# Kernel tuning notes

Measured on AMD Instinct MI355X. Metric: run time of the kernel, lower is better.

The kernel has to match this reference:

```python
import jax, jax.numpy as jnp
import numpy as np

B, F, U, H1, H2 = 2048, 256, 64, 64, 32
E = F + 1  # attention embed dim = num_inputs + 1


def setup_inputs() -> dict:
    key = jax.random.key(0)
    ks = jax.random.split(key, 14)
    s = lambda fan: 1.0 / np.sqrt(fan)
    inp = {
        "x": jax.random.normal(ks[0], (B, F), jnp.float32),
        # stacked per-feature FeatureNN params (Linear(1,U) -> Linear(U,H1) -> Linear(H1,H2) -> Linear(H2,1))
        "w1": jax.random.normal(ks[1], (F, U), jnp.float32) * s(1),
        "b1": jnp.zeros((F, U), jnp.float32),
        "w2": jax.random.normal(ks[2], (F, U, H1), jnp.float32) * s(U),
        "b2": jnp.zeros((F, H1), jnp.float32),
        "w3": jax.random.normal(ks[3], (F, H1, H2), jnp.float32) * s(H1),
        "b3": jnp.zeros((F, H2), jnp.float32),
        "w4": jax.random.normal(ks[4], (F, H2), jnp.float32) * s(H2),
        "b4": jnp.zeros((F,), jnp.float32),
        # MultiheadAttention(E, 1) params: packed qkv in_proj + out_proj
        "in_w": jax.random.normal(ks[5], (3 * E, E), jnp.float32) * s(E),
        "in_b": jnp.zeros((3 * E,), jnp.float32),
        "out_w": jax.random.normal(ks[6], (E, E), jnp.float32) * s(E),
        "out_b": jnp.zeros((E,), jnp.float32),
        "bias": jnp.zeros((1,), jnp.float32),
    }
    return inp


def _attention(x, in_w, in_b, out_w, out_b):
    # x: [B, F]; build [B, F, E] = concat(one-hot feature index, value)
    b = x.shape[0]
    eye = jnp.eye(F, dtype=x.dtype)
    xa = jnp.concatenate([jnp.broadcast_to(eye, (b, F, F)), x[:, :, None]], axis=-1)  # [B,F,E]
    qkv = jnp.einsum("bse,fe->bsf", xa, in_w) + in_b  # [B,F,3E]
    q, k, v = jnp.split(qkv, 3, axis=-1)
    scores = jnp.einsum("bqe,bke->bqk", q, k) / jnp.sqrt(jnp.asarray(E, x.dtype))
    attn = jax.nn.softmax(scores, axis=-1)
    ctx = jnp.einsum("bqk,bke->bqe", attn, v)
    out = jnp.einsum("bqe,fe->bqf", ctx, out_w) + out_b  # out_proj
    return out[:, :, -1]  # keep only the value channel -> [B, F]


def _feature_nns(x, w1, b1, w2, b2, w3, b3, w4, b4):
    # x: [B, F] -> per-feature independent MLPs, batched across features
    h = jax.nn.relu(x[:, :, None] * w1[None] + b1[None])          # [B,F,U]
    h = jax.nn.relu(jnp.einsum("bfu,fuh->bfh", h, w2) + b2[None])  # [B,F,H1]
    h = jax.nn.relu(jnp.einsum("bfh,fhg->bfg", h, w3) + b3[None])  # [B,F,H2]
    return jnp.einsum("bfg,fg->bf", h, w4) + b4[None]              # [B,F]


def reference(x, w1, b1, w2, b2, w3, b3, w4, b4, in_w, in_b, out_w, out_b, bias):
    xa = _attention(x, in_w, in_b, out_w, out_b)                   # att_before_flag=True
    fo = _feature_nns(xa, w1, b1, w2, b2, w3, b3, w4, b4)          # dropout is identity (p=0 / eval)
    out = jnp.sum(fo, axis=-1) + bias                              # [B] + bias -> [B]
    return (out, fo)
```

## Files before the change

kernel.cpp:

```cpp
#include <hip/hip_runtime.h>

#define BB 2048
#define FF 256
#define EE 257
#define UU 64
#define HH1 64
#define HH2 32

#define SC 0.089992807f

typedef __attribute__((ext_vector_type(8))) short short8;
typedef __attribute__((ext_vector_type(4))) float f32x4;
typedef __attribute__((ext_vector_type(4))) unsigned u32x4;
typedef __attribute__((ext_vector_type(2))) unsigned u32x2;

#define MF(a, b, c) __builtin_amdgcn_mfma_f32_16x16x32_bf16(a, b, c, 0, 0, 0)
#define EXP2(x) __builtin_amdgcn_exp2f(x)

__device__ inline unsigned cvt_pk(float a, float b) {
    unsigned r;
    asm("v_cvt_pk_bf16_f32 %0, %1, %2" : "=v"(r) : "v"(a), "v"(b));
    return r;
}
struct HiLo { unsigned hi, lo; };
__device__ inline HiLo split2(float a, float b) {
    HiLo r;
    r.hi = cvt_pk(a, b);
    float ha = __builtin_bit_cast(float, r.hi << 16);
    float hb = __builtin_bit_cast(float, r.hi & 0xFFFF0000u);
    r.lo = cvt_pk(a - ha, b - hb);
    return r;
}

__global__ __launch_bounds__(256) void k_prep(const float* __restrict__ in_w,
                                              const float* __restrict__ in_b,
                                              const float* __restrict__ out_w,
                                              const float* __restrict__ out_b,
                                              const float* __restrict__ w2,
                                              const float* __restrict__ w3,
                                              float* __restrict__ mt,
                                              float* __restrict__ uv, float* __restrict__ wgf,
                                              float* __restrict__ sc,
                                              short* __restrict__ w2s, short* __restrict__ w3s) {
    const int blk = blockIdx.x;
    const int t = threadIdx.x;
    __shared__ float red[4][256];
    __shared__ float s0[EE + 3];
    __shared__ float s1[EE + 3];
    if (blk < 256) {
        const int ki = blk;
        for (int j = t; j < EE; j += 256) {
            s0[j] = in_w[(EE + j) * EE + ki] + in_b[EE + j];
            s1[j] = in_b[j];
        }
        __syncthreads();
        const int w = t >> 6, l = t & 63;
        const int j0 = (w * EE) >> 2, j1 = ((w + 1) * EE) >> 2;
        float acc[4] = {0.f, 0.f, 0.f, 0.f};
#pragma unroll 4
        for (int j = j0; j < j1; ++j) {
            float ak = s0[j];
            float bj = s1[j];
#pragma unroll
            for (int g = 0; g < 4; ++g) {
                float aq = in_w[j * EE + l + 64 * g] + bj;
                acc[g] = fmaf(aq, ak, acc[g]);
            }
        }
#pragma unroll
        for (int g = 0; g < 4; ++g) red[w][l + 64 * g] = acc[g];
        __syncthreads();
        {
            float s = red[0][t] + red[1][t] + red[2][t] + red[3][t];
            mt[(ki >> 1) * 512 + t * 2 + (ki & 1)] = s * SC;
        }
    } else if (blk < 512) {
        const int f = blk - 256;
        const int l = t & 63, q = t >> 6;
        const int lr = l & 15, lq = l >> 4;
        const float* w2f = w2 + f * (UU * HH1);
        const float* w3f = w3 + f * (HH1 * HH2);
        short* o2 = w2s + f * 8192;
        short* o3 = w3s + f * 4096;
        const int hperm = (q & 1) * 32 + (lr >> 2) * 8 + ((q >> 1) << 2) + (lr & 3);
#pragma unroll
        for (int kb = 0; kb < 2; ++kb) {
            float v[8];
#pragma unroll
            for (int j = 0; j < 8; ++j) v[j] = w2f[(kb * 32 + lq * 8 + j) * HH1 + hperm];
            u32x4 hi, lo;
#pragma unroll
            for (int p = 0; p < 4; ++p) {
                HiLo s = split2(v[2 * p], v[2 * p + 1]);
                hi[p] = s.hi; lo[p] = s.lo;
            }
            *(short8*)(o2 + ((0 * 2 + kb) * 4 + q) * 512 + l * 8) = __builtin_bit_cast(short8, hi);
            *(short8*)(o2 + ((1 * 2 + kb) * 4 + q) * 512 + l * 8) = __builtin_bit_cast(short8, lo);
        }
        {
            const int kb = q & 1, ct = q >> 1;
            float v[8];
#pragma unroll
            for (int j = 0; j < 8; ++j) v[j] = w3f[(kb * 32 + lq * 8 + j) * HH2 + ct * 16 + lr];
            u32x4 hi, lo;
#pragma unroll
            for (int p = 0; p < 4; ++p) {
                HiLo s = split2(v[2 * p], v[2 * p + 1]);
                hi[p] = s.hi; lo[p] = s.lo;
            }
            *(short8*)(o3 + ((0 * 2 + kb) * 2 + ct) * 512 + l * 8) = __builtin_bit_cast(short8, hi);
            *(short8*)(o3 + ((1 * 2 + kb) * 2 + ct) * 512 + l * 8) = __builtin_bit_cast(short8, lo);
        }
    } else if (blk < 515) {
        const int which = blk - 512;
        for (int j = t; j < EE; j += 256) {
            if (which == 0)      { s0[j] = in_w[(EE + j) * EE + FF];    s1[j] = in_b[j]; }
            else if (which == 1) { s0[j] = in_w[j * EE + FF];           s1[j] = in_b[EE + j]; }
            else                 { s0[j] = out_w[(EE - 1) * EE + j];    s1[j] = in_b[2 * EE + j]; }
        }
        __syncthreads();
        const int w = t >> 6, l = t & 63;
        const int j0 = (w * EE) >> 2, j1 = ((w + 1) * EE) >> 2;
        const int rowbase = which * EE;
        float acc[4] = {0.f, 0.f, 0.f, 0.f};
#pragma unroll 4
        for (int j = j0; j < j1; ++j) {
            float sk = s0[j];
            float bj = s1[j];
#pragma unroll
            for (int g = 0; g < 4; ++g) {
                float av = in_w[(rowbase + j) * EE + l + 64 * g] + bj;
                acc[g] = fmaf(av, sk, acc[g]);
            }
        }
#pragma unroll
        for (int g = 0; g < 4; ++g) red[w][l + 64 * g] = acc[g];
        __syncthreads();
        {
            float s = red[0][t] + red[1][t] + red[2][t] + red[3][t];
            if (which == 0)      uv[t]          = s * SC;
            else if (which == 1) wgf[2 * t]     = s * SC;
            else                 wgf[2 * t + 1] = s;
        }
    } else {
        const int j = t;
        float cq = in_w[j * EE + FF];
        float ck = in_w[(EE + j) * EE + FF];
        float cv = in_w[(2 * EE + j) * EE + FF];
        float rj = out_w[(EE - 1) * EE + j];
        float pa = cq * ck, pb = cv * rj;
        if (t == 0) {
            const int j2 = 256;
            pa += in_w[j2 * EE + FF] * in_w[(EE + j2) * EE + FF];
            pb += in_w[(2 * EE + j2) * EE + FF] * out_w[(EE - 1) * EE + j2];
        }
#pragma unroll
        for (int o = 32; o > 0; o >>= 1) {
            pa += __shfl_down(pa, o, 64);
            pb += __shfl_down(pb, o, 64);
        }
        if ((t & 63) == 0) { red[0][t >> 6] = pa; red[1][t >> 6] = pb; }
        __syncthreads();
        if (t == 0) {
            pa = red[0][0] + red[0][1] + red[0][2] + red[0][3];
            pb = red[1][0] + red[1][1] + red[1][2] + red[1][3];
            sc[0] = pa * SC;
            sc[1] = pb;
            sc[2] = out_b[EE - 1];
        }
    }
}

__global__ __launch_bounds__(256) void k2_attn(const float* __restrict__ x,
                                               const float2* __restrict__ mt2,
                                               const float* __restrict__ uv,
                                               const float* __restrict__ wg,
                                               const float* __restrict__ sc,
                                               float* __restrict__ xa) {
    const int qi = threadIdx.x;
    const int b0 = blockIdx.x * 2;
    __shared__ __align__(16) float xs0[FF];
    __shared__ __align__(16) float xs1[FF];
    __shared__ __align__(16) float wgs[2 * FF];
    xs0[qi] = x[b0 * FF + qi];
    xs1[qi] = x[(b0 + 1) * FF + qi];
    *(float2*)&wgs[2 * qi] = *(const float2*)&wg[2 * qi];
    const float alpha_s = sc[0], beta = sc[1], ob = sc[2];
    const float uq = uv[qi];
    __syncthreads();
    const float xq0 = xs0[qi];
    const float xq1 = xs1[qi];
    const float a0 = fmaf(alpha_s, xq0, uq);
    const float a1 = fmaf(alpha_s, xq1, uq);
    float le0 = 0.f, le1 = 0.f, p0 = 0.f, p1 = 0.f, q0 = 0.f, q1 = 0.f;
#pragma unroll 8
    for (int kp = 0; kp < FF / 2; ++kp) {
        const float2 m   = mt2[kp * FF + qi];
        const f32x4 wgk  = *(const f32x4*)&wgs[4 * kp];
        const float2 xk0 = *(const float2*)&xs0[2 * kp];
        const float2 xk1 = *(const float2*)&xs1[2 * kp];
        float e;
        e = EXP2(fmaf(xk0.x, a0, fmaf(wgk[0], xq0, m.x))); le0 += e; p0 = fmaf(e, wgk[1], p0); q0 = fmaf(e, xk0.x, q0);
        e = EXP2(fmaf(xk0.y, a0, fmaf(wgk[2], xq0, m.y))); le0 += e; p0 = fmaf(e, wgk[3], p0); q0 = fmaf(e, xk0.y, q0);
        e = EXP2(fmaf(xk1.x, a1, fmaf(wgk[0], xq1, m.x))); le1 += e; p1 = fmaf(e, wgk[1], p1); q1 = fmaf(e, xk1.x, q1);
        e = EXP2(fmaf(xk1.y, a1, fmaf(wgk[2], xq1, m.y))); le1 += e; p1 = fmaf(e, wgk[3], p1); q1 = fmaf(e, xk1.y, q1);
    }
    xa[b0 * FF + qi]       = (p0 + beta * q0) / le0 + ob;
    xa[(b0 + 1) * FF + qi] = (p1 + beta * q1) / le1 + ob;
}

__global__ __launch_bounds__(256, 3) void k3_fnn(const float* xa_in,
                                                 const float* __restrict__ w1,
                                                 const float* __restrict__ b1,
                                                 const float* __restrict__ b2,
                                                 const float* __restrict__ b3,
                                                 const float* __restrict__ w4,
                                                 const float* __restrict__ b4,
                                                 const short* __restrict__ w2s,
                                                 const short* __restrict__ w3s,
                                                 float* fo) {
    const int fidx = blockIdx.x & 255;
    const int f   = ((fidx & 7) << 5) | (fidx >> 3);
    const int rq  = blockIdx.x >> 8;
    const int tid = threadIdx.x;
    const int wv  = tid >> 6;
    const int l   = tid & 63;
    const int lr  = l & 15;
    const int lq  = l >> 4;

    const float* w1f = w1 + f * UU;
    const float* b1f = b1 + f * UU;
    const float* b2f = b2 + f * HH1;
    const float* b3f = b3 + f * HH2;
    const float* w4f = w4 + f * HH2;
    const short* w2sf = w2s + f * 8192;
    const short* w3sf = w3s + f * 4096;
    const float b4v  = b4[f];

    short8 W3h[2][2], W3l[2][2];
#pragma unroll
    for (int ct = 0; ct < 2; ++ct)
#pragma unroll
        for (int kb = 0; kb < 2; ++kb) {
            W3h[ct][kb] = *(const short8*)(w3sf + ((0 * 2 + kb) * 2 + ct) * 512 + l * 8);
            W3l[ct][kb] = *(const short8*)(w3sf + ((1 * 2 + kb) * 2 + ct) * 512 + l * 8);
        }
    f32x4 B3v[2], W4v[2];
#pragma unroll
    for (int ct = 0; ct < 2; ++ct) {
        B3v[ct] = *(const f32x4*)(b3f + ct * 16 + lq * 4);
        W4v[ct] = *(const f32x4*)(w4f + ct * 16 + lq * 4);
    }

    __shared__ __align__(16) short w2l[8192];
#pragma unroll
    for (int i = 0; i < 4; ++i)
        *(short8*)(w2l + (tid * 4 + i) * 8) = *(const short8*)(w2sf + (tid * 4 + i) * 8);
    __syncthreads();

    const int cstart = (rq * 64) / 3;
    const int cend   = ((rq + 1) * 64) / 3;
    int ch = cstart + wv;
    if (ch >= cend) return;
    float xv0 = xa_in[(ch * 32 + lr) * FF + f];
    float xv1 = xa_in[(ch * 32 + 16 + lr) * FF + f];
    for (; ch < cend; ch += 4) {
        const int rows0 = ch * 32;
        float nxv0 = 0.f, nxv1 = 0.f;
        if (ch + 4 < cend) {
            nxv0 = xa_in[((ch + 4) * 32 + lr) * FF + f];
            nxv1 = xa_in[((ch + 4) * 32 + 16 + lr) * FF + f];
        }

        short8 Bh[2][2], Bl[2][2];
#pragma unroll
        for (int kb = 0; kb < 2; ++kb) {
            f32x4 wA = *(const f32x4*)(w1f + kb * 32 + lq * 8);
            f32x4 wB = *(const f32x4*)(w1f + kb * 32 + lq * 8 + 4);
            f32x4 bA = *(const f32x4*)(b1f + kb * 32 + lq * 8);
            f32x4 bB = *(const f32x4*)(b1f + kb * 32 + lq * 8 + 4);
#pragma unroll
            for (int rbt = 0; rbt < 2; ++rbt) {
                const float xv = rbt ? xv1 : xv0;
                float h[8];
#pragma unroll
                for (int j = 0; j < 4; ++j) h[j]     = fmaxf(fmaf(xv, wA[j], bA[j]), 0.f);
#pragma unroll
                for (int j = 0; j < 4; ++j) h[4 + j] = fmaxf(fmaf(xv, wB[j], bB[j]), 0.f);
                u32x4 bh, bl;
#pragma unroll
                for (int p = 0; p < 4; ++p) {
                    HiLo s = split2(h[2 * p], h[2 * p + 1]);
                    bh[p] = s.hi; bl[p] = s.lo;
                }
                Bh[rbt][kb] = __builtin_bit_cast(short8, bh);
                Bl[rbt][kb] = __builtin_bit_cast(short8, bl);
            }
        }

        f32x4 acc[2][4];
#pragma unroll
        for (int ht = 0; ht < 4; ++ht) {
            const short8 W2h0 = *(const short8*)(w2l + (0 * 4 + ht) * 512 + l * 8);
            const short8 W2h1 = *(const short8*)(w2l + (1 * 4 + ht) * 512 + l * 8);
            const short8 W2l0 = *(const short8*)(w2l + (2 * 4 + ht) * 512 + l * 8);
            const short8 W2l1 = *(const short8*)(w2l + (3 * 4 + ht) * 512 + l * 8);
            const f32x4 binit = *(const f32x4*)(b2f + (ht & 1) * 32 + lq * 8 + ((ht >> 1) << 2));
#pragma unroll
            for (int rbt = 0; rbt < 2; ++rbt) {
                f32x4 a = binit;
                a = MF(W2h0, Bh[rbt][0], a);
                a = MF(W2h1, Bh[rbt][1], a);
                a = MF(W2h0, Bl[rbt][0], a);
                a = MF(W2h1, Bl[rbt][1], a);
                a = MF(W2l0, Bh[rbt][0], a);
                a = MF(W2l1, Bh[rbt][1], a);
                acc[rbt][ht] = a;
            }
        }

#pragma unroll
        for (int rbt = 0; rbt < 2; ++rbt) {
            short8 Bh3[2], Bl3[2];
#pragma unroll
            for (int kb = 0; kb < 2; ++kb) {
                float e0 = fmaxf(acc[rbt][kb][0], 0.f),     e1 = fmaxf(acc[rbt][kb][1], 0.f);
                float e2 = fmaxf(acc[rbt][kb][2], 0.f),     e3 = fmaxf(acc[rbt][kb][3], 0.f);
                float e4 = fmaxf(acc[rbt][kb + 2][0], 0.f), e5 = fmaxf(acc[rbt][kb + 2][1], 0.f);
                float e6 = fmaxf(acc[rbt][kb + 2][2], 0.f), e7 = fmaxf(acc[rbt][kb + 2][3], 0.f);
                HiLo p0 = split2(e0, e1), p1 = split2(e2, e3);
                HiLo p2 = split2(e4, e5), p3 = split2(e6, e7);
                u32x4 bh, bl;
                bh[0] = p0.hi; bh[1] = p1.hi; bh[2] = p2.hi; bh[3] = p3.hi;
                bl[0] = p0.lo; bl[1] = p1.lo; bl[2] = p2.lo; bl[3] = p3.lo;
                Bh3[kb] = __builtin_bit_cast(short8, bh);
                Bl3[kb] = __builtin_bit_cast(short8, bl);
            }
            float part = 0.f;
#pragma unroll
            for (int ct = 0; ct < 2; ++ct) {
                f32x4 a2 = B3v[ct];
                a2 = MF(W3h[ct][0], Bh3[0], a2);
                a2 = MF(W3h[ct][1], Bh3[1], a2);
                a2 = MF(W3h[ct][0], Bl3[0], a2);
                a2 = MF(W3h[ct][1], Bl3[1], a2);
                a2 = MF(W3l[ct][0], Bh3[0], a2);
                a2 = MF(W3l[ct][1], Bh3[1], a2);
#pragma unroll
                for (int r = 0; r < 4; ++r)
                    part = fmaf(fmaxf(a2[r], 0.f), W4v[ct][r], part);
            }
            part += __shfl_xor(part, 16, 64);
            part += __shfl_xor(part, 32, 64);
            if (lq == 0)
                fo[(rows0 + rbt * 16 + lr) * FF + f] = part + b4v;
        }

        xv0 = nxv0; xv1 = nxv1;
    }
}

__global__ __launch_bounds__(64) void k4_sum(const float* __restrict__ fo,
                                             const float* __restrict__ bias,
                                             float* __restrict__ out) {
    const int b = blockIdx.x;
    const int t = threadIdx.x;
    const float* r = fo + b * FF;
    float s = r[t] + r[t + 64] + r[t + 128] + r[t + 192];
#pragma unroll
    for (int o = 32; o > 0; o >>= 1) s += __shfl_down(s, o, 64);
    if (t == 0) out[b] = s + bias[0];
}

extern "C" void kernel_launch(void* const* d_in, const int* in_sizes, int n_in,
                              void* d_out, int out_size, void* d_ws, size_t ws_size,
                              hipStream_t stream) {
    const float* x    = (const float*)d_in[0];
    const float* w1   = (const float*)d_in[1];
    const float* b1   = (const float*)d_in[2];
    const float* w2   = (const float*)d_in[3];
    const float* b2   = (const float*)d_in[4];
    const float* w3   = (const float*)d_in[5];
    const float* b3   = (const float*)d_in[6];
    const float* w4   = (const float*)d_in[7];
    const float* b4   = (const float*)d_in[8];
    const float* in_w = (const float*)d_in[9];
    const float* in_b = (const float*)d_in[10];
    const float* out_w= (const float*)d_in[11];
    const float* out_b= (const float*)d_in[12];
    const float* bias = (const float*)d_in[13];

    float* out = (float*)d_out;
    float* fo  = out + BB;
    float* ws  = (float*)d_ws;
    float* mt  = ws;
    float* uvp = ws + 65536;
    float* wgp = ws + 65792;
    float* scp = ws + 66304;
    short* w2s = (short*)(ws + 66560);
    short* w3s = w2s + 256 * 8192;

    k_prep<<<516, 256, 0, stream>>>(in_w, in_b, out_w, out_b, w2, w3,
                                    mt, uvp, wgp, scp, w2s, w3s);
    k2_attn<<<BB / 2, 256, 0, stream>>>(x, (const float2*)mt, uvp, wgp, scp, fo);
    k3_fnn<<<FF * 3, 256, 0, stream>>>(fo, w1, b1, b2, b3, w4, b4, w2s, w3s, fo);
    k4_sum<<<BB, 64, 0, stream>>>(fo, bias, out);
}
```

Measured before the change: 66.73 us.

## Restructure FNN kernel: 4 row splits, split MFMA chains, set wave priority

The feature-MLP kernel now splits each feature's batch into 4 row chunks instead of 3, with a fixed, unrolled 4-chunk loop per wave instead of uneven chunk ranges. Each 16-row tile is processed fully (layer 2 then layer 3) before the next, which lowers live accumulators. The 6-long dependent MFMA chains are split into two independent 3-long chains summed at the end, and s_setprio raises wave priority around the MFMA blocks. The b2 bias is hoisted into registers. The aim is more parallelism and shorter MFMA dependency latency, at the cost of more blocks, each reloading W2 into shared memory.

New measurement: 68.62 us. 2.8% more time.

```diff
diff --git a/kernel.cpp b/kernel.cpp
--- a/kernel.cpp
+++ b/kernel.cpp
@@ -31,6 +31,7 @@
     r.lo = cvt_pk(a - ha, b - hb);
     return r;
 }
+__device__ inline f32x4 zero4() { f32x4 r; r[0]=0.f; r[1]=0.f; r[2]=0.f; r[3]=0.f; return r; }
 
 __global__ __launch_bounds__(256) void k_prep(const float* __restrict__ in_w,
                                               const float* __restrict__ in_b,
@@ -251,6 +252,10 @@
         B3v[ct] = *(const f32x4*)(b3f + ct * 16 + lq * 4);
         W4v[ct] = *(const f32x4*)(w4f + ct * 16 + lq * 4);
     }
+    f32x4 B2v[4];
+#pragma unroll
+    for (int ht = 0; ht < 4; ++ht)
+        B2v[ht] = *(const f32x4*)(b2f + (ht & 1) * 32 + lq * 8 + ((ht >> 1) << 2));
 
     __shared__ __align__(16) short w2l[8192];
 #pragma unroll
@@ -258,30 +263,28 @@
         *(short8*)(w2l + (tid * 4 + i) * 8) = *(const short8*)(w2sf + (tid * 4 + i) * 8);
     __syncthreads();
 
-    const int cstart = (rq * 64) / 3;
-    const int cend   = ((rq + 1) * 64) / 3;
-    int ch = cstart + wv;
-    if (ch >= cend) return;
-    float xv0 = xa_in[(ch * 32 + lr) * FF + f];
-    float xv1 = xa_in[(ch * 32 + 16 + lr) * FF + f];
-    for (; ch < cend; ch += 4) {
-        const int rows0 = ch * 32;
+    const int ch0 = rq * 16 + wv * 4;
+    float xv0 = xa_in[(ch0 * 32 + lr) * FF + f];
+    float xv1 = xa_in[(ch0 * 32 + 16 + lr) * FF + f];
+#pragma unroll
+    for (int c = 0; c < 4; ++c) {
+        const int rows0 = (ch0 + c) * 32;
         float nxv0 = 0.f, nxv1 = 0.f;
-        if (ch + 4 < cend) {
-            nxv0 = xa_in[((ch + 4) * 32 + lr) * FF + f];
-            nxv1 = xa_in[((ch + 4) * 32 + 16 + lr) * FF + f];
-        }
-
-        short8 Bh[2][2], Bl[2][2];
-#pragma unroll
-        for (int kb = 0; kb < 2; ++kb) {
-            f32x4 wA = *(const f32x4*)(w1f + kb * 32 + lq * 8);
-            f32x4 wB = *(const f32x4*)(w1f + kb * 32 + lq * 8 + 4);
-            f32x4 bA = *(const f32x4*)(b1f + kb * 32 + lq * 8);
-            f32x4 bB = *(const f32x4*)(b1f + kb * 32 + lq * 8 + 4);
-#pragma unroll
-            for (int rbt = 0; rbt < 2; ++rbt) {
-                const float xv = rbt ? xv1 : xv0;
+        if (c < 3) {
+            nxv0 = xa_in[(rows0 + 32 + lr) * FF + f];
+            nxv1 = xa_in[(rows0 + 48 + lr) * FF + f];
+        }
+
+#pragma unroll
+        for (int rbt = 0; rbt < 2; ++rbt) {
+            const float xv = rbt ? xv1 : xv0;
+            short8 Bh[2], Bl[2];
+#pragma unroll
+            for (int kb = 0; kb < 2; ++kb) {
+                f32x4 wA = *(const f32x4*)(w1f + kb * 32 + lq * 8);
+                f32x4 wB = *(const f32x4*)(w1f + kb * 32 + lq * 8 + 4);
+                f32x4 bA = *(const f32x4*)(b1f + kb * 32 + lq * 8);
+                f32x4 bB = *(const f32x4*)(b1f + kb * 32 + lq * 8 + 4);
                 float h[8];
 #pragma unroll
                 for (int j = 0; j < 4; ++j) h[j]     = fmaxf(fmaf(xv, wA[j], bA[j]), 0.f);
@@ -293,41 +296,38 @@
                     HiLo s = split2(h[2 * p], h[2 * p + 1]);
                     bh[p] = s.hi; bl[p] = s.lo;
                 }
-                Bh[rbt][kb] = __builtin_bit_cast(short8, bh);
-                Bl[rbt][kb] = __builtin_bit_cast(short8, bl);
-            }
-        }
-
-        f32x4 acc[2][4];
-#pragma unroll
-        for (int ht = 0; ht < 4; ++ht) {
-            const short8 W2h0 = *(const short8*)(w2l + (0 * 4 + ht) * 512 + l * 8);
-            const short8 W2h1 = *(const short8*)(w2l + (1 * 4 + ht) * 512 + l * 8);
-            const short8 W2l0 = *(const short8*)(w2l + (2 * 4 + ht) * 512 + l * 8);
-            const short8 W2l1 = *(const short8*)(w2l + (3 * 4 + ht) * 512 + l * 8);
-            const f32x4 binit = *(const f32x4*)(b2f + (ht & 1) * 32 + lq * 8 + ((ht >> 1) << 2));
-#pragma unroll
-            for (int rbt = 0; rbt < 2; ++rbt) {
-                f32x4 a = binit;
-                a = MF(W2h0, Bh[rbt][0], a);
-                a = MF(W2h1, Bh[rbt][1], a);
-                a = MF(W2h0, Bl[rbt][0], a);
-                a = MF(W2h1, Bl[rbt][1], a);
-                a = MF(W2l0, Bh[rbt][0], a);
-                a = MF(W2l1, Bh[rbt][1], a);
-                acc[rbt][ht] = a;
-            }
-        }
-
-#pragma unroll
-        for (int rbt = 0; rbt < 2; ++rbt) {
+                Bh[kb] = __builtin_bit_cast(short8, bh);
+                Bl[kb] = __builtin_bit_cast(short8, bl);
+            }
+
+            f32x4 acc[4];
+            __builtin_amdgcn_s_setprio(1);
+#pragma unroll
+            for (int ht = 0; ht < 4; ++ht) {
+                const short8 W2h0 = *(const short8*)(w2l + (0 * 4 + ht) * 512 + l * 8);
+                const short8 W2h1 = *(const short8*)(w2l + (1 * 4 + ht) * 512 + l * 8);
+                const short8 W2l0 = *(const short8*)(w2l + (2 * 4 + ht) * 512 + l * 8);
+                const short8 W2l1 = *(const short8*)(w2l + (3 * 4 + ht) * 512 + l * 8);
+                f32x4 a = B2v[ht];
+                a = MF(W2h0, Bh[0], a);
+                a = MF(W2h0, Bl[0], a);
+                a = MF(W2l0, Bh[0], a);
+                f32x4 b_ = zero4();
+                b_ = MF(W2h1, Bh[1], b_);
+                b_ = MF(W2h1, Bl[1], b_);
+                b_ = MF(W2l1, Bh[1], b_);
+#pragma unroll
+                for (int r = 0; r < 4; ++r) acc[ht][r] = a[r] + b_[r];
+            }
+            __builtin_amdgcn_s_setprio(0);
+
             short8 Bh3[2], Bl3[2];
 #pragma unroll
             for (int kb = 0; kb < 2; ++kb) {
-                float e0 = fmaxf(acc[rbt][kb][0], 0.f),     e1 = fmaxf(acc[rbt][kb][1], 0.f);
-                float e2 = fmaxf(acc[rbt][kb][2], 0.f),     e3 = fmaxf(acc[rbt][kb][3], 0.f);
-                float e4 = fmaxf(acc[rbt][kb + 2][0], 0.f), e5 = fmaxf(acc[rbt][kb + 2][1], 0.f);
-                float e6 = fmaxf(acc[rbt][kb + 2][2], 0.f), e7 = fmaxf(acc[rbt][kb + 2][3], 0.f);
+                float e0 = fmaxf(acc[kb][0], 0.f),     e1 = fmaxf(acc[kb][1], 0.f);
+                float e2 = fmaxf(acc[kb][2], 0.f),     e3 = fmaxf(acc[kb][3], 0.f);
+                float e4 = fmaxf(acc[kb + 2][0], 0.f), e5 = fmaxf(acc[kb + 2][1], 0.f);
+                float e6 = fmaxf(acc[kb + 2][2], 0.f), e7 = fmaxf(acc[kb + 2][3], 0.f);
                 HiLo p0 = split2(e0, e1), p1 = split2(e2, e3);
                 HiLo p2 = split2(e4, e5), p3 = split2(e6, e7);
                 u32x4 bh, bl;
@@ -336,20 +336,24 @@
                 Bh3[kb] = __builtin_bit_cast(short8, bh);
                 Bl3[kb] = __builtin_bit_cast(short8, bl);
             }
+
             float part = 0.f;
+            __builtin_amdgcn_s_setprio(1);
 #pragma unroll
             for (int ct = 0; ct < 2; ++ct) {
                 f32x4 a2 = B3v[ct];
                 a2 = MF(W3h[ct][0], Bh3[0], a2);
-                a2 = MF(W3h[ct][1], Bh3[1], a2);
                 a2 = MF(W3h[ct][0], Bl3[0], a2);
-                a2 = MF(W3h[ct][1], Bl3[1], a2);
                 a2 = MF(W3l[ct][0], Bh3[0], a2);
-                a2 = MF(W3l[ct][1], Bh3[1], a2);
+                f32x4 c2 = zero4();
+                c2 = MF(W3h[ct][1], Bh3[1], c2);
+                c2 = MF(W3h[ct][1], Bl3[1], c2);
+                c2 = MF(W3l[ct][1], Bh3[1], c2);
 #pragma unroll
                 for (int r = 0; r < 4; ++r)
-                    part = fmaf(fmaxf(a2[r], 0.f), W4v[ct][r], part);
-            }
+                    part = fmaf(fmaxf(a2[r] + c2[r], 0.f), W4v[ct][r], part);
+            }
+            __builtin_amdgcn_s_setprio(0);
             part += __shfl_xor(part, 16, 64);
             part += __shfl_xor(part, 32, 64);
             if (lq == 0)
@@ -403,6 +407,6 @@
     k_prep<<<516, 256, 0, stream>>>(in_w, in_b, out_w, out_b, w2, w3,
                                     mt, uvp, wgp, scp, w2s, w3s);
     k2_attn<<<BB / 2, 256, 0, stream>>>(x, (const float2*)mt, uvp, wgp, scp, fo);
-    k3_fnn<<<FF * 3, 256, 0, stream>>>(fo, w1, b1, b2, b3, w4, b4, w2s, w3s, fo);
+    k3_fnn<<<FF * 4, 256, 0, stream>>>(fo, w1, b1, b2, b3, w4, b4, w2s, w3s, fo);
     k4_sum<<<BB, 64, 0, stream>>>(fo, bias, out);
 }
```

## Widen attention score loads to float4 and split MFMA accumulation chains

Applied to the files above, without the earlier changes.

The precomputed score matrix is re-laid out in groups of four keys, so the attention kernel loads float4 per thread and processes four keys per iteration instead of two. In the feature-MLP kernel, each six-MFMA dependent accumulation chain is split into two independent three-MFMA chains that are summed afterwards, shortening MFMA dependency latency. The b2 bias vectors are also hoisted out of the loop into registers. These changes trade more registers for fewer dependent stalls, which may reduce occupancy.

Result: slower. 69.28 us (+3.8%).

```diff
diff --git a/kernel.cpp b/kernel.cpp
--- a/kernel.cpp
+++ b/kernel.cpp
@@ -31,6 +31,7 @@
     r.lo = cvt_pk(a - ha, b - hb);
     return r;
 }
+__device__ inline f32x4 zero4() { f32x4 r; r[0]=0.f; r[1]=0.f; r[2]=0.f; r[3]=0.f; return r; }
 
 __global__ __launch_bounds__(256) void k_prep(const float* __restrict__ in_w,
                                               const float* __restrict__ in_b,
@@ -72,7 +73,7 @@
         __syncthreads();
         {
             float s = red[0][t] + red[1][t] + red[2][t] + red[3][t];
-            mt[(ki >> 1) * 512 + t * 2 + (ki & 1)] = s * SC;
+            mt[(ki >> 2) * 1024 + t * 4 + (ki & 3)] = s * SC;
         }
     } else if (blk < 512) {
         const int f = blk - 256;
@@ -172,7 +173,7 @@
 }
 
 __global__ __launch_bounds__(256) void k2_attn(const float* __restrict__ x,
-                                               const float2* __restrict__ mt2,
+                                               const float* __restrict__ mt,
                                                const float* __restrict__ uv,
                                                const float* __restrict__ wg,
                                                const float* __restrict__ sc,
@@ -193,17 +194,22 @@
     const float a0 = fmaf(alpha_s, xq0, uq);
     const float a1 = fmaf(alpha_s, xq1, uq);
     float le0 = 0.f, le1 = 0.f, p0 = 0.f, p1 = 0.f, q0 = 0.f, q1 = 0.f;
-#pragma unroll 8
-    for (int kp = 0; kp < FF / 2; ++kp) {
-        const float2 m   = mt2[kp * FF + qi];
-        const f32x4 wgk  = *(const f32x4*)&wgs[4 * kp];
-        const float2 xk0 = *(const float2*)&xs0[2 * kp];
-        const float2 xk1 = *(const float2*)&xs1[2 * kp];
+#pragma unroll 4
+    for (int kq = 0; kq < FF / 4; ++kq) {
+        const f32x4 m   = *(const f32x4*)&mt[kq * 1024 + qi * 4];
+        const f32x4 wgA = *(const f32x4*)&wgs[8 * kq];
+        const f32x4 wgB = *(const f32x4*)&wgs[8 * kq + 4];
+        const f32x4 xk0 = *(const f32x4*)&xs0[4 * kq];
+        const f32x4 xk1 = *(const f32x4*)&xs1[4 * kq];
         float e;
-        e = EXP2(fmaf(xk0.x, a0, fmaf(wgk[0], xq0, m.x))); le0 += e; p0 = fmaf(e, wgk[1], p0); q0 = fmaf(e, xk0.x, q0);
-        e = EXP2(fmaf(xk0.y, a0, fmaf(wgk[2], xq0, m.y))); le0 += e; p0 = fmaf(e, wgk[3], p0); q0 = fmaf(e, xk0.y, q0);
-        e = EXP2(fmaf(xk1.x, a1, fmaf(wgk[0], xq1, m.x))); le1 += e; p1 = fmaf(e, wgk[1], p1); q1 = fmaf(e, xk1.x, q1);
-        e = EXP2(fmaf(xk1.y, a1, fmaf(wgk[2], xq1, m.y))); le1 += e; p1 = fmaf(e, wgk[3], p1); q1 = fmaf(e, xk1.y, q1);
+        e = EXP2(fmaf(xk0[0], a0, fmaf(wgA[0], xq0, m[0]))); le0 += e; p0 = fmaf(e, wgA[1], p0); q0 = fmaf(e, xk0[0], q0);
+        e = EXP2(fmaf(xk0[1], a0, fmaf(wgA[2], xq0, m[1]))); le0 += e; p0 = fmaf(e, wgA[3], p0); q0 = fmaf(e, xk0[1], q0);
+        e = EXP2(fmaf(xk0[2], a0, fmaf(wgB[0], xq0, m[2]))); le0 += e; p0 = fmaf(e, wgB[1], p0); q0 = fmaf(e, xk0[2], q0);
+        e = EXP2(fmaf(xk0[3], a0, fmaf(wgB[2], xq0, m[3]))); le0 += e; p0 = fmaf(e, wgB[3], p0); q0 = fmaf(e, xk0[3], q0);
+        e = EXP2(fmaf(xk1[0], a1, fmaf(wgA[0], xq1, m[0]))); le1 += e; p1 = fmaf(e, wgA[1], p1); q1 = fmaf(e, xk1[0], q1);
+        e = EXP2(fmaf(xk1[1], a1, fmaf(wgA[2], xq1, m[1]))); le1 += e; p1 = fmaf(e, wgA[3], p1); q1 = fmaf(e, xk1[1], q1);
+        e = EXP2(fmaf(xk1[2], a1, fmaf(wgB[0], xq1, m[2]))); le1 += e; p1 = fmaf(e, wgB[1], p1); q1 = fmaf(e, xk1[2], q1);
+        e = EXP2(fmaf(xk1[3], a1, fmaf(wgB[2], xq1, m[3]))); le1 += e; p1 = fmaf(e, wgB[3], p1); q1 = fmaf(e, xk1[3], q1);
     }
     xa[b0 * FF + qi]       = (p0 + beta * q0) / le0 + ob;
     xa[(b0 + 1) * FF + qi] = (p1 + beta * q1) / le1 + ob;
@@ -251,6 +257,10 @@
         B3v[ct] = *(const f32x4*)(b3f + ct * 16 + lq * 4);
         W4v[ct] = *(const f32x4*)(w4f + ct * 16 + lq * 4);
     }
+    f32x4 B2v[4];
+#pragma unroll
+    for (int ht = 0; ht < 4; ++ht)
+        B2v[ht] = *(const f32x4*)(b2f + (ht & 1) * 32 + lq * 8 + ((ht >> 1) << 2));
 
     __shared__ __align__(16) short w2l[8192];
 #pragma unroll
@@ -305,17 +315,18 @@
             const short8 W2h1 = *(const short8*)(w2l + (1 * 4 + ht) * 512 + l * 8);
             const short8 W2l0 = *(const short8*)(w2l + (2 * 4 + ht) * 512 + l * 8);
             const short8 W2l1 = *(const short8*)(w2l + (3 * 4 + ht) * 512 + l * 8);
-            const f32x4 binit = *(const f32x4*)(b2f + (ht & 1) * 32 + lq * 8 + ((ht >> 1) << 2));
 #pragma unroll
             for (int rbt = 0; rbt < 2; ++rbt) {
-                f32x4 a = binit;
+                f32x4 a = B2v[ht];
                 a = MF(W2h0, Bh[rbt][0], a);
-                a = MF(W2h1, Bh[rbt][1], a);
                 a = MF(W2h0, Bl[rbt][0], a);
-                a = MF(W2h1, Bl[rbt][1], a);
                 a = MF(W2l0, Bh[rbt][0], a);
-                a = MF(W2l1, Bh[rbt][1], a);
-                acc[rbt][ht] = a;
+                f32x4 b_ = zero4();
+                b_ = MF(W2h1, Bh[rbt][1], b_);
+                b_ = MF(W2h1, Bl[rbt][1], b_);
+                b_ = MF(W2l1, Bh[rbt][1], b_);
+#pragma unroll
+                for (int r = 0; r < 4; ++r) acc[rbt][ht][r] = a[r] + b_[r];
             }
         }
 
@@ -341,14 +352,15 @@
             for (int ct = 0; ct < 2; ++ct) {
                 f32x4 a2 = B3v[ct];
                 a2 = MF(W3h[ct][0], Bh3[0], a2);
-                a2 = MF(W3h[ct][1], Bh3[1], a2);
                 a2 = MF(W3h[ct][0], Bl3[0], a2);
-                a2 = MF(W3h[ct][1], Bl3[1], a2);
                 a2 = MF(W3l[ct][0], Bh3[0], a2);
-                a2 = MF(W3l[ct][1], Bh3[1], a2);
+                f32x4 c2 = zero4();
+                c2 = MF(W3h[ct][1], Bh3[1], c2);
+                c2 = MF(W3h[ct][1], Bl3[1], c2);
+                c2 = MF(W3l[ct][1], Bh3[1], c2);
 #pragma unroll
                 for (int r = 0; r < 4; ++r)
-                    part = fmaf(fmaxf(a2[r], 0.f), W4v[ct][r], part);
+                    part = fmaf(fmaxf(a2[r] + c2[r], 0.f), W4v[ct][r], part);
             }
             part += __shfl_xor(part, 16, 64);
             part += __shfl_xor(part, 32, 64);
@@ -402,7 +414,7 @@
 
     k_prep<<<516, 256, 0, stream>>>(in_w, in_b, out_w, out_b, w2, w3,
                                     mt, uvp, wgp, scp, w2s, w3s);
-    k2_attn<<<BB / 2, 256, 0, stream>>>(x, (const float2*)mt, uvp, wgp, scp, fo);
+    k2_attn<<<BB / 2, 256, 0, stream>>>(x, mt, uvp, wgp, scp, fo);
     k3_fnn<<<FF * 3, 256, 0, stream>>>(fo, w1, b1, b2, b3, w4, b4, w2s, w3s, fo);
     k4_sum<<<BB, 64, 0, stream>>>(fo, bias, out);
 }
```

## Software-pipeline FNN kernel with double-buffered accumulators and hoisted weights

Applied to the files above, without the earlier changes.

Restructures k3_fnn so each wave processes a fixed 8 chunks. The layer-2 MFMA build for the next chunk is interleaved with the layer-3 epilogue of the previous one, using two accumulator sets. Per-feature w1/b1/b2 loads are hoisted into registers out of the loop. The grid shrinks from 3 to 2 row-groups per feature, with occupancy hint 2, to make room for the extra registers. The aim is to hide MFMA and load latency, at the cost of lower occupancy and one redundant build on the final iteration.

After: 66.65 us. No clear change (-0.1%).

```diff
diff --git a/kernel.cpp b/kernel.cpp
--- a/kernel.cpp
+++ b/kernel.cpp
@@ -209,7 +209,7 @@
     xa[(b0 + 1) * FF + qi] = (p1 + beta * q1) / le1 + ob;
 }
 
-__global__ __launch_bounds__(256, 3) void k3_fnn(const float* xa_in,
+__global__ __launch_bounds__(256, 2) void k3_fnn(const float* xa_in,
                                                  const float* __restrict__ w1,
                                                  const float* __restrict__ b1,
                                                  const float* __restrict__ b2,
@@ -221,7 +221,7 @@
                                                  float* fo) {
     const int fidx = blockIdx.x & 255;
     const int f   = ((fidx & 7) << 5) | (fidx >> 3);
-    const int rq  = blockIdx.x >> 8;
+    const int rh  = blockIdx.x >> 8;
     const int tid = threadIdx.x;
     const int wv  = tid >> 6;
     const int l   = tid & 63;
@@ -251,6 +251,18 @@
         B3v[ct] = *(const f32x4*)(b3f + ct * 16 + lq * 4);
         W4v[ct] = *(const f32x4*)(w4f + ct * 16 + lq * 4);
     }
+    f32x4 B2v[4];
+#pragma unroll
+    for (int ht = 0; ht < 4; ++ht)
+        B2v[ht] = *(const f32x4*)(b2f + (ht & 1) * 32 + lq * 8 + ((ht >> 1) << 2));
+    f32x4 W1v[2], W1w[2], B1v[2], B1w[2];
+#pragma unroll
+    for (int kb = 0; kb < 2; ++kb) {
+        W1v[kb] = *(const f32x4*)(w1f + kb * 32 + lq * 8);
+        W1w[kb] = *(const f32x4*)(w1f + kb * 32 + lq * 8 + 4);
+        B1v[kb] = *(const f32x4*)(b1f + kb * 32 + lq * 8);
+        B1w[kb] = *(const f32x4*)(b1f + kb * 32 + lq * 8 + 4);
+    }
 
     __shared__ __align__(16) short w2l[8192];
 #pragma unroll
@@ -258,35 +270,18 @@
         *(short8*)(w2l + (tid * 4 + i) * 8) = *(const short8*)(w2sf + (tid * 4 + i) * 8);
     __syncthreads();
 
-    const int cstart = (rq * 64) / 3;
-    const int cend   = ((rq + 1) * 64) / 3;
-    int ch = cstart + wv;
-    if (ch >= cend) return;
-    float xv0 = xa_in[(ch * 32 + lr) * FF + f];
-    float xv1 = xa_in[(ch * 32 + 16 + lr) * FF + f];
-    for (; ch < cend; ch += 4) {
-        const int rows0 = ch * 32;
-        float nxv0 = 0.f, nxv1 = 0.f;
-        if (ch + 4 < cend) {
-            nxv0 = xa_in[((ch + 4) * 32 + lr) * FF + f];
-            nxv1 = xa_in[((ch + 4) * 32 + 16 + lr) * FF + f];
-        }
-
+    auto BUILD = [&](f32x4 (&acc)[2][4], float xv0, float xv1) {
         short8 Bh[2][2], Bl[2][2];
 #pragma unroll
         for (int kb = 0; kb < 2; ++kb) {
-            f32x4 wA = *(const f32x4*)(w1f + kb * 32 + lq * 8);
-            f32x4 wB = *(const f32x4*)(w1f + kb * 32 + lq * 8 + 4);
-            f32x4 bA = *(const f32x4*)(b1f + kb * 32 + lq * 8);
-            f32x4 bB = *(const f32x4*)(b1f + kb * 32 + lq * 8 + 4);
 #pragma unroll
             for (int rbt = 0; rbt < 2; ++rbt) {
                 const float xv = rbt ? xv1 : xv0;
                 float h[8];
 #pragma unroll
-                for (int j = 0; j < 4; ++j) h[j]     = fmaxf(fmaf(xv, wA[j], bA[j]), 0.f);
-#pragma unroll
-                for (int j = 0; j < 4; ++j) h[4 + j] = fmaxf(fmaf(xv, wB[j], bB[j]), 0.f);
+                for (int j = 0; j < 4; ++j) h[j]     = fmaxf(fmaf(xv, W1v[kb][j], B1v[kb][j]), 0.f);
+#pragma unroll
+                for (int j = 0; j < 4; ++j) h[4 + j] = fmaxf(fmaf(xv, W1w[kb][j], B1w[kb][j]), 0.f);
                 u32x4 bh, bl;
 #pragma unroll
                 for (int p = 0; p < 4; ++p) {
@@ -297,18 +292,15 @@
                 Bl[rbt][kb] = __builtin_bit_cast(short8, bl);
             }
         }
-
-        f32x4 acc[2][4];
 #pragma unroll
         for (int ht = 0; ht < 4; ++ht) {
             const short8 W2h0 = *(const short8*)(w2l + (0 * 4 + ht) * 512 + l * 8);
             const short8 W2h1 = *(const short8*)(w2l + (1 * 4 + ht) * 512 + l * 8);
             const short8 W2l0 = *(const short8*)(w2l + (2 * 4 + ht) * 512 + l * 8);
             const short8 W2l1 = *(const short8*)(w2l + (3 * 4 + ht) * 512 + l * 8);
-            const f32x4 binit = *(const f32x4*)(b2f + (ht & 1) * 32 + lq * 8 + ((ht >> 1) << 2));
 #pragma unroll
             for (int rbt = 0; rbt < 2; ++rbt) {
-                f32x4 a = binit;
+                f32x4 a = B2v[ht];
                 a = MF(W2h0, Bh[rbt][0], a);
                 a = MF(W2h1, Bh[rbt][1], a);
                 a = MF(W2h0, Bl[rbt][0], a);
@@ -318,7 +310,10 @@
                 acc[rbt][ht] = a;
             }
         }
-
+    };
+
+    auto EPI = [&](f32x4 (&acc)[2][4], int ch) {
+        const int rows0 = ch * 32;
 #pragma unroll
         for (int rbt = 0; rbt < 2; ++rbt) {
             short8 Bh3[2], Bl3[2];
@@ -355,8 +350,28 @@
             if (lq == 0)
                 fo[(rows0 + rbt * 16 + lr) * FF + f] = part + b4v;
         }
-
-        xv0 = nxv0; xv1 = nxv1;
+    };
+
+    const int ch0 = rh * 32 + wv * 8;
+    f32x4 accA[2][4], accB[2][4];
+    float xa0 = xa_in[(ch0 * 32 + lr) * FF + f];
+    float xa1 = xa_in[(ch0 * 32 + 16 + lr) * FF + f];
+    float xb0 = xa_in[((ch0 + 1) * 32 + lr) * FF + f];
+    float xb1 = xa_in[((ch0 + 1) * 32 + 16 + lr) * FF + f];
+    BUILD(accA, xa0, xa1);
+    for (int i = 0; i < 4; ++i) {
+        const int chA = ch0 + 2 * i;
+        const int c2 = (2 * i + 2 < 8) ? chA + 2 : chA;
+        const int c3 = (2 * i + 3 < 8) ? chA + 3 : chA;
+        const float n0 = xa_in[(c2 * 32 + lr) * FF + f];
+        const float n1 = xa_in[(c2 * 32 + 16 + lr) * FF + f];
+        BUILD(accB, xb0, xb1);
+        EPI(accA, chA);
+        const float m0 = xa_in[(c3 * 32 + lr) * FF + f];
+        const float m1 = xa_in[(c3 * 32 + 16 + lr) * FF + f];
+        BUILD(accA, n0, n1);
+        EPI(accB, chA + 1);
+        xb0 = m0; xb1 = m1;
     }
 }
 
@@ -403,6 +418,6 @@
     k_prep<<<516, 256, 0, stream>>>(in_w, in_b, out_w, out_b, w2, w3,
                                     mt, uvp, wgp, scp, w2s, w3s);
     k2_attn<<<BB / 2, 256, 0, stream>>>(x, (const float2*)mt, uvp, wgp, scp, fo);
-    k3_fnn<<<FF * 3, 256, 0, stream>>>(fo, w1, b1, b2, b3, w4, b4, w2s, w3s, fo);
+    k3_fnn<<<FF * 2, 256, 0, stream>>>(fo, w1, b1, b2, b3, w4, b4, w2s, w3s, fo);
     k4_sum<<<BB, 64, 0, stream>>>(fo, bias, out);
 }
```
